# Performance work log

Hardware: AMD Instinct MI355X
Metric: run time of the kernel (lower is better)

Reference implementation:

```python
import jax, jax.numpy as jnp
import numpy as np

B, H, S, D = 4, 8, 2048, 64

def setup_inputs() -> dict:
    key = jax.random.key(0)
    k1, k2 = jax.random.split(key)
    q = jax.random.normal(k1, (B, H, S, D), dtype=jnp.float32)
    kv = jax.random.normal(k2, (B, H, S, D), dtype=jnp.float32)
    mask = jnp.zeros((1, 1, S, S), dtype=jnp.float32)
    return {"q": q, "kv": kv, "mask": mask}

def reference(q, kv, mask):
    # score = q @ kv^T / sqrt(d_k) + mask ; softmax over last dim ; @ kv
    d_k = jnp.asarray(kv.shape[-1], dtype=q.dtype)
    score = jnp.einsum('bhqd,bhkd->bhqk', q, kv) / jnp.sqrt(d_k)
    score = score + mask
    attn = jax.nn.softmax(score, axis=-1)
    out = jnp.einsum('bhqk,bhkd->bhqd', attn, kv)
    return out
```

## Files before the change

### kernel.cpp

```cpp
#include <hip/hip_runtime.h>
#include <hip/hip_bf16.h>
#include <stdint.h>


typedef __bf16 bf16;
typedef __attribute__((ext_vector_type(8))) __bf16 bf16x8;
typedef __attribute__((ext_vector_type(4))) __bf16 bf16x4;
typedef __attribute__((ext_vector_type(4))) float floatx4;
typedef __attribute__((ext_vector_type(16))) float floatx16;
typedef __attribute__((ext_vector_type(4))) int int4v;
typedef __attribute__((ext_vector_type(2))) unsigned int uint2v;

#define SLEN 2048
#define DH   64
#define BR   64
#define BC   64
#define NKT  (SLEN / BC)
#define NEP  (NKT / 2)
#define NQT  (SLEN / BR)
#define BH_N 32
#define LOG2E 1.44269504088896341f

#define CHB_L  1024
#define IMGB_L 8192
#define IMGE_G 4096
#define BUF2   (4 * IMGB_L)

#define AS1 __attribute__((address_space(1)))
#define AS3 __attribute__((address_space(3)))

static __device__ inline void gload_lds16(const void* g, void* l) {
    __builtin_amdgcn_global_load_lds((const AS1 uint32_t*)g, (AS3 uint32_t*)l, 16, 0, 0);
}

static __device__ inline float fexp2(float x) {
    return __builtin_amdgcn_exp2f(x);
}

static_assert(BH_N == NQT, "prep kernel folds bh and qt onto one grid axis");

__global__ __launch_bounds__(256) void kv_prep(
    const float* __restrict__ kv, const float* __restrict__ mask,
    bf16* __restrict__ kvK, bf16* __restrict__ kvT, int* __restrict__ flags)
{
    __shared__ bf16 Tl[64 * 72];
    __shared__ int wany[4];
    const int kt = blockIdx.x, z = blockIdx.y;
    const int t = threadIdx.x;

    float acc = 0.f;
#pragma unroll
    for (int i = 0; i < 4; ++i) {
        int f = i * 256 + t;
        int row = f >> 4, c4 = (f & 15) * 4;
        const float4 v = *(const float4*)(mask + (size_t)(z * BR + row) * SLEN + kt * BC + c4);
        acc = fmaxf(acc, fmaxf(fmaxf(fabsf(v.x), fabsf(v.y)), fmaxf(fabsf(v.z), fabsf(v.w))));
    }
    unsigned long long any = __ballot(acc != 0.f);
    if ((t & 63) == 0) wany[t >> 6] = (any != 0ull) ? 1 : 0;

    const float* src = kv + ((size_t)z * SLEN + kt * BC) * DH;
#pragma unroll
    for (int i = 0; i < 4; ++i) {
        int f = i * 256 + t;
        int key = f >> 4, d4 = (f & 15) * 4;
        float4 v = *(const float4*)(src + (size_t)key * DH + d4);
        bf16x4 b; b[0] = (bf16)v.x; b[1] = (bf16)v.y; b[2] = (bf16)v.z; b[3] = (bf16)v.w;
        *(bf16x4*)&Tl[key * 72 + d4] = b;
    }
    __syncthreads();
    if (t == 0) flags[z * NKT + kt] = wany[0] | wany[1] | wany[2] | wany[3];

    bf16* outK = kvK + ((size_t)z * NKT + kt) * IMGE_G;
#pragma unroll
    for (int i = 0; i < 2; ++i) {
        int G = i * 256 + t;
        int c = G >> 6, L = G & 63, rl = L >> 3, p = L & 7;
        int g = (p - rl - 4 * (c & 1)) & 7, key = 8 * c + rl;
        bf16x8 w = *(const bf16x8*)&Tl[key * 72 + g * 8];
        *(bf16x8*)(outK + (size_t)G * 8) = w;
    }
    bf16* outV = kvT + ((size_t)z * NKT + kt) * IMGE_G;
#pragma unroll
    for (int i = 0; i < 2; ++i) {
        int G = i * 256 + t;
        int c = G >> 6, L = G & 63, dl = L >> 3, p = L & 7;
        int g = (p - dl - 4 * (c & 1)) & 7, d = 8 * c + dl;
        bf16x8 w;
#pragma unroll
        for (int j = 0; j < 8; ++j)
            w[j] = Tl[(8 * g + j) * 72 + d];
        *(bf16x8*)(outV + (size_t)G * 8) = w;
    }
}

__global__ __launch_bounds__(256, 2) void attn_fwd16(
    const float* __restrict__ q, const float* __restrict__ mask,
    const int* __restrict__ flags,
    const bf16* __restrict__ kvK, const bf16* __restrict__ kvT,
    float* __restrict__ out)
{
    __shared__ __align__(16) char smem[2 * BUF2];

    const int bh = blockIdx.x;
    const int qt = blockIdx.y;
    const int q0 = qt * 128;
    const int t = threadIdx.x;
    const int w = t >> 6, lane = t & 63;
    const int r5 = lane & 31, h = lane >> 5;
    const int c3 = r5 >> 3, rl = lane & 7;

    const float qscale = 0.125f * LOG2E;
    bf16x8 qf[4];
    {
        const float* qrow = q + ((size_t)bh * SLEN + q0 + w * 32 + r5) * DH;
#pragma unroll
        for (int s = 0; s < 4; ++s) {
            float4 f0 = *(const float4*)(qrow + 16 * s + 8 * h);
            float4 f1 = *(const float4*)(qrow + 16 * s + 8 * h + 4);
            bf16x8 a;
            a[0] = (bf16)(f0.x * qscale); a[1] = (bf16)(f0.y * qscale);
            a[2] = (bf16)(f0.z * qscale); a[3] = (bf16)(f0.w * qscale);
            a[4] = (bf16)(f1.x * qscale); a[5] = (bf16)(f1.y * qscale);
            a[6] = (bf16)(f1.z * qscale); a[7] = (bf16)(f1.w * qscale);
            qf[s] = a;
        }
    }

    const int fqt = qt * 2 + (w >> 1);
    unsigned fmask;
    {
        int ld = (lane < 32) ? flags[fqt * NKT + lane] : 0;
        fmask = (unsigned)__ballot(ld != 0);
    }

    int addr4[4];
#pragma unroll
    for (int s = 0; s < 4; ++s) {
        int slot = (2 * s + h + rl + 4 * (c3 & 1)) & 7;
        addr4[s] = c3 * 1024 + rl * 128 + slot * 16;
    }

    floatx16 o[2];
#pragma unroll
    for (int dt = 0; dt < 2; ++dt)
#pragma unroll
        for (int i = 0; i < 16; ++i) o[dt][i] = 0.f;
    float l_run = 0.f;

    const bf16* kvKb = kvK + (size_t)bh * NKT * IMGE_G;
    const bf16* kvTb = kvT + (size_t)bh * NKT * IMGE_G;

    auto stage = [&](int t2, char* Bn) {
        const bf16* gK = kvKb + (size_t)t2 * IMGE_G;
        const bf16* gV = kvTb + (size_t)t2 * IMGE_G;
#pragma unroll
        for (int cc = 0; cc < 2; ++cc) {
            const int c = 2 * w + cc;
            gload_lds16(gK + (size_t)c * 512 + lane * 8,          Bn +              c * CHB_L);
            gload_lds16(gV + (size_t)c * 512 + lane * 8,          Bn + IMGB_L +     c * CHB_L);
            gload_lds16(gK + IMGE_G + (size_t)c * 512 + lane * 8, Bn + 2 * IMGB_L + c * CHB_L);
            gload_lds16(gV + IMGE_G + (size_t)c * 512 + lane * 8, Bn + 3 * IMGB_L + c * CHB_L);
        }
    };

    stage(0, smem);

    for (int e = 0; e < NEP; ++e) {
        __syncthreads();

        if (e + 1 < NEP) stage(2 * e + 2, smem + ((e + 1) & 1) * BUF2);

        const char* B = smem + (e & 1) * BUF2;

        floatx16 s[4];
#pragma unroll
        for (int T = 0; T < 4; ++T) {
            const char* Kimg = B + (T >> 1) * (2 * IMGB_L) + (T & 1) * 4096;
            floatx16 acc;
#pragma unroll
            for (int i = 0; i < 16; ++i) acc[i] = 0.f;
#pragma unroll
            for (int ss = 0; ss < 4; ++ss) {
                bf16x8 kf = *(const bf16x8*)(Kimg + addr4[ss]);
                acc = __builtin_amdgcn_mfma_f32_32x32x16_bf16(kf, qf[ss], acc, 0, 0, 0);
            }
            s[T] = acc;
        }

#pragma unroll
        for (int T = 0; T < 4; ++T) {
            if (fmask & (1u << (2 * e + (T >> 1)))) {
                const float* mrow = mask + (size_t)(q0 + w * 32 + r5) * SLEN
                                    + e * 128 + T * 32 + 4 * h;
#pragma unroll
                for (int g4 = 0; g4 < 4; ++g4) {
                    float4 mv = *(const float4*)(mrow + 8 * g4);
                    s[T][4 * g4 + 0] += mv.x * LOG2E;
                    s[T][4 * g4 + 1] += mv.y * LOG2E;
                    s[T][4 * g4 + 2] += mv.z * LOG2E;
                    s[T][4 * g4 + 3] += mv.w * LOG2E;
                }
            }
        }

        float rs = 0.f;
#pragma unroll
        for (int T = 0; T < 4; ++T) {
            float ev[16];
#pragma unroll
            for (int i = 0; i < 16; ++i) ev[i] = fexp2(s[T][i]);
            float r0 = (ev[0] + ev[1]) + (ev[2] + ev[3]);
            float r1 = (ev[4] + ev[5]) + (ev[6] + ev[7]);
            float r2 = (ev[8] + ev[9]) + (ev[10] + ev[11]);
            float r3 = (ev[12] + ev[13]) + (ev[14] + ev[15]);
            rs += (r0 + r1) + (r2 + r3);

            bf16x4 lA = { (bf16)ev[0],  (bf16)ev[1],  (bf16)ev[2],  (bf16)ev[3]  };
            bf16x4 hA = { (bf16)ev[4],  (bf16)ev[5],  (bf16)ev[6],  (bf16)ev[7]  };
            bf16x4 lB = { (bf16)ev[8],  (bf16)ev[9],  (bf16)ev[10], (bf16)ev[11] };
            bf16x4 hB = { (bf16)ev[12], (bf16)ev[13], (bf16)ev[14], (bf16)ev[15] };
            uint2v xA = __builtin_bit_cast(uint2v, lA);
            uint2v yA = __builtin_bit_cast(uint2v, hA);
            uint2v xB = __builtin_bit_cast(uint2v, lB);
            uint2v yB = __builtin_bit_cast(uint2v, hB);
            uint2v sA0 = __builtin_amdgcn_permlane32_swap(xA[0], yA[0], false, false);
            uint2v sA1 = __builtin_amdgcn_permlane32_swap(xA[1], yA[1], false, false);
            uint2v sB0 = __builtin_amdgcn_permlane32_swap(xB[0], yB[0], false, false);
            uint2v sB1 = __builtin_amdgcn_permlane32_swap(xB[1], yB[1], false, false);
            int4v pAi = { (int)sA0[0], (int)sA1[0], (int)sA0[1], (int)sA1[1] };
            int4v pBi = { (int)sB0[0], (int)sB1[0], (int)sB0[1], (int)sB1[1] };
            bf16x8 pfA = __builtin_bit_cast(bf16x8, pAi);
            bf16x8 pfB = __builtin_bit_cast(bf16x8, pBi);

            const char* Vimg = B + IMGB_L + (T >> 1) * (2 * IMGB_L);
            const int uA = 2 * (T & 1), uB = uA + 1;
#pragma unroll
            for (int dt = 0; dt < 2; ++dt) {
                bf16x8 vA = *(const bf16x8*)(Vimg + dt * 4096 + addr4[uA]);
                o[dt] = __builtin_amdgcn_mfma_f32_32x32x16_bf16(vA, pfA, o[dt], 0, 0, 0);
                bf16x8 vB = *(const bf16x8*)(Vimg + dt * 4096 + addr4[uB]);
                o[dt] = __builtin_amdgcn_mfma_f32_32x32x16_bf16(vB, pfB, o[dt], 0, 0, 0);
            }
        }
        l_run += rs;
    }

    float l = l_run + __shfl_xor(l_run, 32);
    const float inv = 1.0f / l;
    float* ob = out + ((size_t)bh * SLEN + q0 + w * 32 + r5) * DH + 4 * h;
#pragma unroll
    for (int dt = 0; dt < 2; ++dt)
#pragma unroll
        for (int k = 0; k < 4; ++k) {
            float4 v;
            v.x = o[dt][4 * k + 0] * inv;
            v.y = o[dt][4 * k + 1] * inv;
            v.z = o[dt][4 * k + 2] * inv;
            v.w = o[dt][4 * k + 3] * inv;
            *(float4*)(ob + dt * 32 + 8 * k) = v;
        }
}

#define LDT 72
__global__ __launch_bounds__(256) void attn_mask_flags(
    const float* __restrict__ mask, int* __restrict__ flags)
{
    const int kt = blockIdx.x, qt = blockIdx.y;
    const int t = threadIdx.x;
    float acc = 0.f;
#pragma unroll
    for (int i = 0; i < 4; ++i) {
        int f = i * 256 + t;
        int row = f >> 4, c4 = (f & 15) * 4;
        const float4 v = *(const float4*)(mask + (size_t)(qt * BR + row) * SLEN + kt * BC + c4);
        acc = fmaxf(acc, fmaxf(fmaxf(fabsf(v.x), fabsf(v.y)), fmaxf(fabsf(v.z), fabsf(v.w))));
    }
    unsigned long long any = __ballot(acc != 0.f);
    __shared__ int wany[4];
    if ((t & 63) == 0) wany[t >> 6] = (any != 0ull) ? 1 : 0;
    __syncthreads();
    if (t == 0) flags[qt * NKT + kt] = wany[0] | wany[1] | wany[2] | wany[3];
}

__global__ __launch_bounds__(256) void attn_fwd(
    const float* __restrict__ q, const float* __restrict__ kv,
    const float* __restrict__ mask, const int* __restrict__ flags,
    float* __restrict__ out)
{
    __shared__ __align__(16) bf16 Kl[BC * LDT];
    __shared__ __align__(16) bf16 Vt[DH * LDT];
    __shared__ __align__(16) bf16 Pl[BR * LDT];

    const int qt = blockIdx.x;
    const int bh = blockIdx.y;
    const int q0 = qt * BR;
    const int t = threadIdx.x;
    const int wave = t >> 6, lane = t & 63;
    const int ln16 = lane & 15, quad = lane >> 4;

    const float qscale = 0.125f * LOG2E;
    bf16x8 aq[2];
    {
        const float* qrow = q + ((size_t)bh * SLEN + q0 + wave * 16 + ln16) * DH;
#pragma unroll
        for (int kc = 0; kc < 2; ++kc) {
            float4 f0 = *(const float4*)(qrow + kc * 32 + quad * 8);
            float4 f1 = *(const float4*)(qrow + kc * 32 + quad * 8 + 4);
            bf16x8 a;
            a[0] = (bf16)(f0.x * qscale); a[1] = (bf16)(f0.y * qscale);
            a[2] = (bf16)(f0.z * qscale); a[3] = (bf16)(f0.w * qscale);
            a[4] = (bf16)(f1.x * qscale); a[5] = (bf16)(f1.y * qscale);
            a[6] = (bf16)(f1.z * qscale); a[7] = (bf16)(f1.w * qscale);
            aq[kc] = a;
        }
    }

    floatx4 o[4];
#pragma unroll
    for (int dt = 0; dt < 4; ++dt) o[dt] = (floatx4){0.f, 0.f, 0.f, 0.f};
    float m_run[4], l_run[4];
#pragma unroll
    for (int r = 0; r < 4; ++r) { m_run[r] = -3.0e38f; l_run[r] = 0.f; }

    const float* kvb = kv + (size_t)bh * SLEN * DH;

    for (int kt = 0; kt < NKT; ++kt) {
        float4 st[4];
        const float* kvt = kvb + (size_t)kt * BC * DH;
#pragma unroll
        for (int i = 0; i < 4; ++i) {
            int f = i * 256 + t;
            st[i] = *(const float4*)(kvt + (size_t)f * 4);
        }
        __syncthreads();
#pragma unroll
        for (int i = 0; i < 4; ++i) {
            int f = i * 256 + t;
            int key = f >> 4, d4 = (f & 15) * 4;
            bf16 b0 = (bf16)st[i].x, b1 = (bf16)st[i].y, b2 = (bf16)st[i].z, b3 = (bf16)st[i].w;
            *(bf16x4*)&Kl[key * LDT + d4] = (bf16x4){b0, b1, b2, b3};
            Vt[(d4 + 0) * LDT + key] = b0;
            Vt[(d4 + 1) * LDT + key] = b1;
            Vt[(d4 + 2) * LDT + key] = b2;
            Vt[(d4 + 3) * LDT + key] = b3;
        }
        __syncthreads();

        floatx4 s[4];
#pragma unroll
        for (int nt = 0; nt < 4; ++nt) {
            s[nt] = (floatx4){0.f, 0.f, 0.f, 0.f};
#pragma unroll
            for (int kc = 0; kc < 2; ++kc) {
                bf16x8 bk = *(const bf16x8*)&Kl[(ln16 + 16 * nt) * LDT + kc * 32 + quad * 8];
                s[nt] = __builtin_amdgcn_mfma_f32_16x16x32_bf16(aq[kc], bk, s[nt], 0, 0, 0);
            }
        }

        if (!flags || flags[qt * NKT + kt]) {
            const float* mrow = mask + (size_t)(q0 + quad * 4) * SLEN + kt * BC + ln16;
#pragma unroll
            for (int r = 0; r < 4; ++r)
#pragma unroll
                for (int nt = 0; nt < 4; ++nt)
                    s[nt][r] += mrow[(size_t)r * SLEN + nt * 16] * LOG2E;
        }

#pragma unroll
        for (int r = 0; r < 4; ++r) {
            float mx = fmaxf(fmaxf(s[0][r], s[1][r]), fmaxf(s[2][r], s[3][r]));
            mx = fmaxf(mx, __shfl_xor(mx, 1));
            mx = fmaxf(mx, __shfl_xor(mx, 2));
            mx = fmaxf(mx, __shfl_xor(mx, 4));
            mx = fmaxf(mx, __shfl_xor(mx, 8));
            float mnew = fmaxf(m_run[r], mx);
            float alpha = exp2f(m_run[r] - mnew);
            m_run[r] = mnew;
            float rs = 0.f;
#pragma unroll
            for (int nt = 0; nt < 4; ++nt) {
                float p = exp2f(s[nt][r] - mnew);
                s[nt][r] = p;
                rs += p;
            }
            rs += __shfl_xor(rs, 1);
            rs += __shfl_xor(rs, 2);
            rs += __shfl_xor(rs, 4);
            rs += __shfl_xor(rs, 8);
            l_run[r] = l_run[r] * alpha + rs;
#pragma unroll
            for (int dt = 0; dt < 4; ++dt) o[dt][r] *= alpha;
        }

#pragma unroll
        for (int nt = 0; nt < 4; ++nt)
#pragma unroll
            for (int r = 0; r < 4; ++r)
                Pl[(wave * 16 + quad * 4 + r) * LDT + ln16 + 16 * nt] = (bf16)s[nt][r];

#pragma unroll
        for (int kc2 = 0; kc2 < 2; ++kc2) {
            bf16x8 pfr = *(const bf16x8*)&Pl[(wave * 16 + ln16) * LDT + kc2 * 32 + quad * 8];
#pragma unroll
            for (int dt = 0; dt < 4; ++dt) {
                bf16x8 vfr = *(const bf16x8*)&Vt[(ln16 + 16 * dt) * LDT + kc2 * 32 + quad * 8];
                o[dt] = __builtin_amdgcn_mfma_f32_16x16x32_bf16(pfr, vfr, o[dt], 0, 0, 0);
            }
        }
    }

#pragma unroll
    for (int r = 0; r < 4; ++r) {
        float inv = 1.0f / l_run[r];
        int qrow = q0 + wave * 16 + quad * 4 + r;
        float* orow = out + ((size_t)bh * SLEN + qrow) * DH;
#pragma unroll
        for (int dt = 0; dt < 4; ++dt)
            orow[ln16 + 16 * dt] = o[dt][r] * inv;
    }
}

extern "C" void kernel_launch(void* const* d_in, const int* in_sizes, int n_in,
                              void* d_out, int out_size, void* d_ws, size_t ws_size,
                              hipStream_t stream)
{
    const float* q    = (const float*)d_in[0];
    const float* kv   = (const float*)d_in[1];
    const float* mask = (const float*)d_in[2];
    float* out = (float*)d_out;

    const size_t kvKoff = 4096;
    const size_t kvToff = kvKoff + (size_t)BH_N * NKT * IMGE_G * 2;
    const size_t need   = kvToff + (size_t)BH_N * NKT * IMGE_G * 2;

    if (ws_size >= need) {
        int*  flags = (int*)d_ws;
        bf16* kvK   = (bf16*)((char*)d_ws + kvKoff);
        bf16* kvT   = (bf16*)((char*)d_ws + kvToff);
        kv_prep<<<dim3(NKT, BH_N), 256, 0, stream>>>(kv, mask, kvK, kvT, flags);
        attn_fwd16<<<dim3(BH_N, SLEN / 128), 256, 0, stream>>>(q, mask, flags, kvK, kvT, out);
    } else {
        int* flags = nullptr;
        if (ws_size >= (size_t)NQT * NKT * sizeof(int)) {
            flags = (int*)d_ws;
            attn_mask_flags<<<dim3(NKT, NQT), 256, 0, stream>>>(mask, flags);
        }
        attn_fwd<<<dim3(NQT, BH_N), 256, 0, stream>>>(q, kv, mask, flags, out);
    }
}
```

Baseline: 133.1 us.

## Split key tiles across warp pairs, each warp covering 64 query rows, reduce via LDS

Each warp now handles 64 query rows (two 32-row groups) but only one of the two 64-key tiles per stage, instead of 32 query rows over both key tiles. Every K and V fragment read from LDS now feeds two MFMAs, halving LDS read traffic per MFMA. The partial outputs and row sums of the two key-half warps are combined through shared memory at the end. The cost is more accumulator registers (four output tiles plus doubled scores) under the 2-blocks-per-SM launch bound, and an extra LDS reduction with barriers.

```diff
diff --git a/kernel.cpp b/kernel.cpp
--- a/kernel.cpp
+++ b/kernel.cpp
@@ -94,7 +94,7 @@
     }
 }
 
-__global__ __launch_bounds__(256, 2) void attn_fwd16(
+__global__ __launch_bounds__(256, 2) void attn_fwd17(
     const float* __restrict__ q, const float* __restrict__ mask,
     const int* __restrict__ flags,
     const bf16* __restrict__ kvK, const bf16* __restrict__ kvT,
@@ -107,13 +107,15 @@
     const int q0 = qt * 128;
     const int t = threadIdx.x;
     const int w = t >> 6, lane = t & 63;
+    const int kh = w & 1, qh = w >> 1;
     const int r5 = lane & 31, h = lane >> 5;
     const int c3 = r5 >> 3, rl = lane & 7;
 
     const float qscale = 0.125f * LOG2E;
-    bf16x8 qf[4];
-    {
-        const float* qrow = q + ((size_t)bh * SLEN + q0 + w * 32 + r5) * DH;
+    bf16x8 qf[2][4];
+#pragma unroll
+    for (int g = 0; g < 2; ++g) {
+        const float* qrow = q + ((size_t)bh * SLEN + q0 + qh * 64 + g * 32 + r5) * DH;
 #pragma unroll
         for (int s = 0; s < 4; ++s) {
             float4 f0 = *(const float4*)(qrow + 16 * s + 8 * h);
@@ -123,11 +125,11 @@
             a[2] = (bf16)(f0.z * qscale); a[3] = (bf16)(f0.w * qscale);
             a[4] = (bf16)(f1.x * qscale); a[5] = (bf16)(f1.y * qscale);
             a[6] = (bf16)(f1.z * qscale); a[7] = (bf16)(f1.w * qscale);
-            qf[s] = a;
-        }
-    }
-
-    const int fqt = qt * 2 + (w >> 1);
+            qf[g][s] = a;
+        }
+    }
+
+    const int fqt = qt * 2 + qh;
     unsigned fmask;
     {
         int ld = (lane < 32) ? flags[fqt * NKT + lane] : 0;
@@ -141,12 +143,14 @@
         addr4[s] = c3 * 1024 + rl * 128 + slot * 16;
     }
 
-    floatx16 o[2];
-#pragma unroll
-    for (int dt = 0; dt < 2; ++dt)
-#pragma unroll
-        for (int i = 0; i < 16; ++i) o[dt][i] = 0.f;
-    float l_run = 0.f;
+    floatx16 o[2][2];
+#pragma unroll
+    for (int g = 0; g < 2; ++g)
+#pragma unroll
+        for (int dt = 0; dt < 2; ++dt)
+#pragma unroll
+            for (int i = 0; i < 16; ++i) o[g][dt][i] = 0.f;
+    float l_run[2] = {0.f, 0.f};
 
     const bf16* kvKb = kvK + (size_t)bh * NKT * IMGE_G;
     const bf16* kvTb = kvT + (size_t)bh * NKT * IMGE_G;
@@ -171,95 +175,142 @@
 
         if (e + 1 < NEP) stage(2 * e + 2, smem + ((e + 1) & 1) * BUF2);
 
-        const char* B = smem + (e & 1) * BUF2;
-
-        floatx16 s[4];
-#pragma unroll
-        for (int T = 0; T < 4; ++T) {
-            const char* Kimg = B + (T >> 1) * (2 * IMGB_L) + (T & 1) * 4096;
-            floatx16 acc;
-#pragma unroll
-            for (int i = 0; i < 16; ++i) acc[i] = 0.f;
+        const char* B    = smem + (e & 1) * BUF2;
+        const char* Kimg = B + kh * (2 * IMGB_L);
+        const char* Vimg = B + IMGB_L + kh * (2 * IMGB_L);
+        const int   ktile = 2 * e + kh;
+        const bool  domask = (fmask >> ktile) & 1u;
+
+#pragma unroll
+        for (int T = 0; T < 2; ++T) {
+            floatx16 s0, s1;
+#pragma unroll
+            for (int i = 0; i < 16; ++i) { s0[i] = 0.f; s1[i] = 0.f; }
 #pragma unroll
             for (int ss = 0; ss < 4; ++ss) {
-                bf16x8 kf = *(const bf16x8*)(Kimg + addr4[ss]);
-                acc = __builtin_amdgcn_mfma_f32_32x32x16_bf16(kf, qf[ss], acc, 0, 0, 0);
-            }
-            s[T] = acc;
-        }
-
-#pragma unroll
-        for (int T = 0; T < 4; ++T) {
-            if (fmask & (1u << (2 * e + (T >> 1)))) {
-                const float* mrow = mask + (size_t)(q0 + w * 32 + r5) * SLEN
-                                    + e * 128 + T * 32 + 4 * h;
+                bf16x8 kf = *(const bf16x8*)(Kimg + T * 4096 + addr4[ss]);
+                s0 = __builtin_amdgcn_mfma_f32_32x32x16_bf16(kf, qf[0][ss], s0, 0, 0, 0);
+                s1 = __builtin_amdgcn_mfma_f32_32x32x16_bf16(kf, qf[1][ss], s1, 0, 0, 0);
+            }
+
+            if (domask) {
+                const float* m0 = mask + (size_t)(q0 + qh * 64 + r5) * SLEN
+                                  + ktile * 64 + T * 32 + 4 * h;
+                const float* m1 = m0 + (size_t)32 * SLEN;
 #pragma unroll
                 for (int g4 = 0; g4 < 4; ++g4) {
-                    float4 mv = *(const float4*)(mrow + 8 * g4);
-                    s[T][4 * g4 + 0] += mv.x * LOG2E;
-                    s[T][4 * g4 + 1] += mv.y * LOG2E;
-                    s[T][4 * g4 + 2] += mv.z * LOG2E;
-                    s[T][4 * g4 + 3] += mv.w * LOG2E;
+                    float4 a = *(const float4*)(m0 + 8 * g4);
+                    float4 b = *(const float4*)(m1 + 8 * g4);
+                    s0[4 * g4 + 0] += a.x * LOG2E; s0[4 * g4 + 1] += a.y * LOG2E;
+                    s0[4 * g4 + 2] += a.z * LOG2E; s0[4 * g4 + 3] += a.w * LOG2E;
+                    s1[4 * g4 + 0] += b.x * LOG2E; s1[4 * g4 + 1] += b.y * LOG2E;
+                    s1[4 * g4 + 2] += b.z * LOG2E; s1[4 * g4 + 3] += b.w * LOG2E;
                 }
             }
-        }
-
-        float rs = 0.f;
-#pragma unroll
-        for (int T = 0; T < 4; ++T) {
-            float ev[16];
-#pragma unroll
-            for (int i = 0; i < 16; ++i) ev[i] = fexp2(s[T][i]);
-            float r0 = (ev[0] + ev[1]) + (ev[2] + ev[3]);
-            float r1 = (ev[4] + ev[5]) + (ev[6] + ev[7]);
-            float r2 = (ev[8] + ev[9]) + (ev[10] + ev[11]);
-            float r3 = (ev[12] + ev[13]) + (ev[14] + ev[15]);
-            rs += (r0 + r1) + (r2 + r3);
-
-            bf16x4 lA = { (bf16)ev[0],  (bf16)ev[1],  (bf16)ev[2],  (bf16)ev[3]  };
-            bf16x4 hA = { (bf16)ev[4],  (bf16)ev[5],  (bf16)ev[6],  (bf16)ev[7]  };
-            bf16x4 lB = { (bf16)ev[8],  (bf16)ev[9],  (bf16)ev[10], (bf16)ev[11] };
-            bf16x4 hB = { (bf16)ev[12], (bf16)ev[13], (bf16)ev[14], (bf16)ev[15] };
-            uint2v xA = __builtin_bit_cast(uint2v, lA);
-            uint2v yA = __builtin_bit_cast(uint2v, hA);
-            uint2v xB = __builtin_bit_cast(uint2v, lB);
-            uint2v yB = __builtin_bit_cast(uint2v, hB);
-            uint2v sA0 = __builtin_amdgcn_permlane32_swap(xA[0], yA[0], false, false);
-            uint2v sA1 = __builtin_amdgcn_permlane32_swap(xA[1], yA[1], false, false);
-            uint2v sB0 = __builtin_amdgcn_permlane32_swap(xB[0], yB[0], false, false);
-            uint2v sB1 = __builtin_amdgcn_permlane32_swap(xB[1], yB[1], false, false);
-            int4v pAi = { (int)sA0[0], (int)sA1[0], (int)sA0[1], (int)sA1[1] };
-            int4v pBi = { (int)sB0[0], (int)sB1[0], (int)sB0[1], (int)sB1[1] };
-            bf16x8 pfA = __builtin_bit_cast(bf16x8, pAi);
-            bf16x8 pfB = __builtin_bit_cast(bf16x8, pBi);
-
-            const char* Vimg = B + IMGB_L + (T >> 1) * (2 * IMGB_L);
-            const int uA = 2 * (T & 1), uB = uA + 1;
+
+            float ev0[16], ev1[16];
+#pragma unroll
+            for (int i = 0; i < 16; ++i) { ev0[i] = fexp2(s0[i]); ev1[i] = fexp2(s1[i]); }
+            l_run[0] += ((ev0[0] + ev0[1]) + (ev0[2] + ev0[3]))
+                      + ((ev0[4] + ev0[5]) + (ev0[6] + ev0[7]))
+                      + ((ev0[8] + ev0[9]) + (ev0[10] + ev0[11]))
+                      + ((ev0[12] + ev0[13]) + (ev0[14] + ev0[15]));
+            l_run[1] += ((ev1[0] + ev1[1]) + (ev1[2] + ev1[3]))
+                      + ((ev1[4] + ev1[5]) + (ev1[6] + ev1[7]))
+                      + ((ev1[8] + ev1[9]) + (ev1[10] + ev1[11]))
+                      + ((ev1[12] + ev1[13]) + (ev1[14] + ev1[15]));
+
+            bf16x8 pf0A, pf0B, pf1A, pf1B;
+            {
+                bf16x4 lA = { (bf16)ev0[0],  (bf16)ev0[1],  (bf16)ev0[2],  (bf16)ev0[3]  };
+                bf16x4 hA = { (bf16)ev0[4],  (bf16)ev0[5],  (bf16)ev0[6],  (bf16)ev0[7]  };
+                bf16x4 lB = { (bf16)ev0[8],  (bf16)ev0[9],  (bf16)ev0[10], (bf16)ev0[11] };
+                bf16x4 hB = { (bf16)ev0[12], (bf16)ev0[13], (bf16)ev0[14], (bf16)ev0[15] };
+                uint2v xA = __builtin_bit_cast(uint2v, lA);
+                uint2v yA = __builtin_bit_cast(uint2v, hA);
+                uint2v xB = __builtin_bit_cast(uint2v, lB);
+                uint2v yB = __builtin_bit_cast(uint2v, hB);
+                uint2v sA0 = __builtin_amdgcn_permlane32_swap(xA[0], yA[0], false, false);
+                uint2v sA1 = __builtin_amdgcn_permlane32_swap(xA[1], yA[1], false, false);
+                uint2v sB0 = __builtin_amdgcn_permlane32_swap(xB[0], yB[0], false, false);
+                uint2v sB1 = __builtin_amdgcn_permlane32_swap(xB[1], yB[1], false, false);
+                int4v pAi = { (int)sA0[0], (int)sA1[0], (int)sA0[1], (int)sA1[1] };
+                int4v pBi = { (int)sB0[0], (int)sB1[0], (int)sB0[1], (int)sB1[1] };
+                pf0A = __builtin_bit_cast(bf16x8, pAi);
+                pf0B = __builtin_bit_cast(bf16x8, pBi);
+            }
+            {
+                bf16x4 lA = { (bf16)ev1[0],  (bf16)ev1[1],  (bf16)ev1[2],  (bf16)ev1[3]  };
+                bf16x4 hA = { (bf16)ev1[4],  (bf16)ev1[5],  (bf16)ev1[6],  (bf16)ev1[7]  };
+                bf16x4 lB = { (bf16)ev1[8],  (bf16)ev1[9],  (bf16)ev1[10], (bf16)ev1[11] };
+                bf16x4 hB = { (bf16)ev1[12], (bf16)ev1[13], (bf16)ev1[14], (bf16)ev1[15] };
+                uint2v xA = __builtin_bit_cast(uint2v, lA);
+                uint2v yA = __builtin_bit_cast(uint2v, hA);
+                uint2v xB = __builtin_bit_cast(uint2v, lB);
+                uint2v yB = __builtin_bit_cast(uint2v, hB);
+                uint2v sA0 = __builtin_amdgcn_permlane32_swap(xA[0], yA[0], false, false);
+                uint2v sA1 = __builtin_amdgcn_permlane32_swap(xA[1], yA[1], false, false);
+                uint2v sB0 = __builtin_amdgcn_permlane32_swap(xB[0], yB[0], false, false);
+                uint2v sB1 = __builtin_amdgcn_permlane32_swap(xB[1], yB[1], false, false);
+                int4v pAi = { (int)sA0[0], (int)sA1[0], (int)sA0[1], (int)sA1[1] };
+                int4v pBi = { (int)sB0[0], (int)sB1[0], (int)sB0[1], (int)sB1[1] };
+                pf1A = __builtin_bit_cast(bf16x8, pAi);
+                pf1B = __builtin_bit_cast(bf16x8, pBi);
+            }
+
+            const int uA = 2 * T, uB = 2 * T + 1;
 #pragma unroll
             for (int dt = 0; dt < 2; ++dt) {
                 bf16x8 vA = *(const bf16x8*)(Vimg + dt * 4096 + addr4[uA]);
-                o[dt] = __builtin_amdgcn_mfma_f32_32x32x16_bf16(vA, pfA, o[dt], 0, 0, 0);
                 bf16x8 vB = *(const bf16x8*)(Vimg + dt * 4096 + addr4[uB]);
-                o[dt] = __builtin_amdgcn_mfma_f32_32x32x16_bf16(vB, pfB, o[dt], 0, 0, 0);
-            }
-        }
-        l_run += rs;
-    }
-
-    float l = l_run + __shfl_xor(l_run, 32);
-    const float inv = 1.0f / l;
-    float* ob = out + ((size_t)bh * SLEN + q0 + w * 32 + r5) * DH + 4 * h;
-#pragma unroll
-    for (int dt = 0; dt < 2; ++dt)
-#pragma unroll
-        for (int k = 0; k < 4; ++k) {
-            float4 v;
-            v.x = o[dt][4 * k + 0] * inv;
-            v.y = o[dt][4 * k + 1] * inv;
-            v.z = o[dt][4 * k + 2] * inv;
-            v.w = o[dt][4 * k + 3] * inv;
-            *(float4*)(ob + dt * 32 + 8 * k) = v;
-        }
+                o[0][dt] = __builtin_amdgcn_mfma_f32_32x32x16_bf16(vA, pf0A, o[0][dt], 0, 0, 0);
+                o[0][dt] = __builtin_amdgcn_mfma_f32_32x32x16_bf16(vB, pf0B, o[0][dt], 0, 0, 0);
+                o[1][dt] = __builtin_amdgcn_mfma_f32_32x32x16_bf16(vA, pf1A, o[1][dt], 0, 0, 0);
+                o[1][dt] = __builtin_amdgcn_mfma_f32_32x32x16_bf16(vB, pf1B, o[1][dt], 0, 0, 0);
+            }
+        }
+    }
+
+    __syncthreads();
+    float* Obuf = (float*)smem;
+    float* Lbuf = (float*)(smem + 32768);
+    if (kh == 1) {
+#pragma unroll
+        for (int g = 0; g < 2; ++g) {
+#pragma unroll
+            for (int dt = 0; dt < 2; ++dt)
+#pragma unroll
+                for (int k = 0; k < 4; ++k) {
+                    float4 v;
+                    v.x = o[g][dt][4 * k + 0]; v.y = o[g][dt][4 * k + 1];
+                    v.z = o[g][dt][4 * k + 2]; v.w = o[g][dt][4 * k + 3];
+                    *(float4*)(Obuf + ((size_t)(((qh * 2 + g) * 2 + dt) * 4 + k) * 64 + lane) * 4) = v;
+                }
+            Lbuf[(qh * 2 + g) * 64 + lane] = l_run[g];
+        }
+    }
+    __syncthreads();
+    if (kh == 0) {
+#pragma unroll
+        for (int g = 0; g < 2; ++g) {
+            float lsum = l_run[g] + Lbuf[(qh * 2 + g) * 64 + lane];
+            float l = lsum + __shfl_xor(lsum, 32);
+            float inv = 1.f / l;
+            float* ob = out + ((size_t)bh * SLEN + q0 + qh * 64 + g * 32 + r5) * DH + 4 * h;
+#pragma unroll
+            for (int dt = 0; dt < 2; ++dt)
+#pragma unroll
+                for (int k = 0; k < 4; ++k) {
+                    float4 p = *(const float4*)(Obuf + ((size_t)(((qh * 2 + g) * 2 + dt) * 4 + k) * 64 + lane) * 4);
+                    float4 v;
+                    v.x = (o[g][dt][4 * k + 0] + p.x) * inv;
+                    v.y = (o[g][dt][4 * k + 1] + p.y) * inv;
+                    v.z = (o[g][dt][4 * k + 2] + p.z) * inv;
+                    v.w = (o[g][dt][4 * k + 3] + p.w) * inv;
+                    *(float4*)(ob + dt * 32 + 8 * k) = v;
+                }
+        }
+    }
 }
 
 #define LDT 72
@@ -439,7 +490,7 @@
         bf16* kvK   = (bf16*)((char*)d_ws + kvKoff);
         bf16* kvT   = (bf16*)((char*)d_ws + kvToff);
         kv_prep<<<dim3(NKT, BH_N), 256, 0, stream>>>(kv, mask, kvK, kvT, flags);
-        attn_fwd16<<<dim3(BH_N, SLEN / 128), 256, 0, stream>>>(q, mask, flags, kvK, kvT, out);
+        attn_fwd17<<<dim3(BH_N, SLEN / 128), 256, 0, stream>>>(q, mask, flags, kvK, kvT, out);
     } else {
         int* flags = nullptr;
         if (ws_size >= (size_t)NQT * NKT * sizeof(int)) {
```

Measured after the change: 133.7 us. Within noise of the previous version (+0.5%).

## Split KV range across two wave groups, load fragments directly from global

Applied to the files above, without the earlier changes.

The attention kernel now uses 512 threads, with two groups of four waves each covering half of the key tiles for the same query rows. It drops the LDS double-buffered staging and instead reads K/V fragments straight from global memory, using a new prep layout that matches the MFMA operand order. Partial outputs and row sums are combined through shared memory at the end. The aim is more waves in flight to hide latency and no LDS staging or barriers per tile, at the cost of uncoalesced-by-LDS global reads relying on cache and an extra reduction step.

```diff
diff --git a/kernel.cpp b/kernel.cpp
--- a/kernel.cpp
+++ b/kernel.cpp
@@ -16,22 +16,14 @@
 #define BR   64
 #define BC   64
 #define NKT  (SLEN / BC)
-#define NEP  (NKT / 2)
 #define NQT  (SLEN / BR)
 #define BH_N 32
 #define LOG2E 1.44269504088896341f
 
-#define CHB_L  1024
-#define IMGB_L 8192
 #define IMGE_G 4096
-#define BUF2   (4 * IMGB_L)
 
 #define AS1 __attribute__((address_space(1)))
 #define AS3 __attribute__((address_space(3)))
-
-static __device__ inline void gload_lds16(const void* g, void* l) {
-    __builtin_amdgcn_global_load_lds((const AS1 uint32_t*)g, (AS3 uint32_t*)l, 16, 0, 0);
-}
 
 static __device__ inline float fexp2(float x) {
     return __builtin_amdgcn_exp2f(x);
@@ -75,45 +67,46 @@
 #pragma unroll
     for (int i = 0; i < 2; ++i) {
         int G = i * 256 + t;
-        int c = G >> 6, L = G & 63, rl = L >> 3, p = L & 7;
-        int g = (p - rl - 4 * (c & 1)) & 7, key = 8 * c + rl;
-        bf16x8 w = *(const bf16x8*)&Tl[key * 72 + g * 8];
+        int u = G >> 8, ss = (G >> 6) & 3, ln = G & 63;
+        int key = u * 32 + (ln & 31), d0 = 16 * ss + 8 * (ln >> 5);
+        bf16x8 w = *(const bf16x8*)&Tl[key * 72 + d0];
         *(bf16x8*)(outK + (size_t)G * 8) = w;
     }
     bf16* outV = kvT + ((size_t)z * NKT + kt) * IMGE_G;
 #pragma unroll
     for (int i = 0; i < 2; ++i) {
         int G = i * 256 + t;
-        int c = G >> 6, L = G & 63, dl = L >> 3, p = L & 7;
-        int g = (p - dl - 4 * (c & 1)) & 7, d = 8 * c + dl;
+        int dt = G >> 8, u = (G >> 7) & 1, ff = (G >> 6) & 1, ln = G & 63;
+        int d = dt * 32 + (ln & 31), kb = u * 32 + 16 * ff + 8 * (ln >> 5);
         bf16x8 w;
 #pragma unroll
         for (int j = 0; j < 8; ++j)
-            w[j] = Tl[(8 * g + j) * 72 + d];
+            w[j] = Tl[(kb + j) * 72 + d];
         *(bf16x8*)(outV + (size_t)G * 8) = w;
     }
 }
 
-__global__ __launch_bounds__(256, 2) void attn_fwd16(
+__global__ __launch_bounds__(512, 2) void attn_fwd19(
     const float* __restrict__ q, const float* __restrict__ mask,
     const int* __restrict__ flags,
     const bf16* __restrict__ kvK, const bf16* __restrict__ kvT,
     float* __restrict__ out)
 {
-    __shared__ __align__(16) char smem[2 * BUF2];
+    __shared__ __align__(16) float Obuf[4 * 2 * 4 * 64 * 4];
+    __shared__ float Lbuf[4 * 64];
 
     const int bh = blockIdx.x;
     const int qt = blockIdx.y;
     const int q0 = qt * 128;
     const int t = threadIdx.x;
     const int w = t >> 6, lane = t & 63;
+    const int qg = w & 3, kh = w >> 2;
     const int r5 = lane & 31, h = lane >> 5;
-    const int c3 = r5 >> 3, rl = lane & 7;
 
     const float qscale = 0.125f * LOG2E;
     bf16x8 qf[4];
     {
-        const float* qrow = q + ((size_t)bh * SLEN + q0 + w * 32 + r5) * DH;
+        const float* qrow = q + ((size_t)bh * SLEN + q0 + qg * 32 + r5) * DH;
 #pragma unroll
         for (int s = 0; s < 4; ++s) {
             float4 f0 = *(const float4*)(qrow + 16 * s + 8 * h);
@@ -127,20 +120,13 @@
         }
     }
 
-    const int fqt = qt * 2 + (w >> 1);
+    const int fqt = qt * 2 + (qg >> 1);
     unsigned fmask;
     {
         int ld = (lane < 32) ? flags[fqt * NKT + lane] : 0;
         fmask = (unsigned)__ballot(ld != 0);
     }
 
-    int addr4[4];
-#pragma unroll
-    for (int s = 0; s < 4; ++s) {
-        int slot = (2 * s + h + rl + 4 * (c3 & 1)) & 7;
-        addr4[s] = c3 * 1024 + rl * 128 + slot * 16;
-    }
-
     floatx16 o[2];
 #pragma unroll
     for (int dt = 0; dt < 2; ++dt)
@@ -148,78 +134,62 @@
         for (int i = 0; i < 16; ++i) o[dt][i] = 0.f;
     float l_run = 0.f;
 
-    const bf16* kvKb = kvK + (size_t)bh * NKT * IMGE_G;
-    const bf16* kvTb = kvT + (size_t)bh * NKT * IMGE_G;
-
-    auto stage = [&](int t2, char* Bn) {
-        const bf16* gK = kvKb + (size_t)t2 * IMGE_G;
-        const bf16* gV = kvTb + (size_t)t2 * IMGE_G;
-#pragma unroll
-        for (int cc = 0; cc < 2; ++cc) {
-            const int c = 2 * w + cc;
-            gload_lds16(gK + (size_t)c * 512 + lane * 8,          Bn +              c * CHB_L);
-            gload_lds16(gV + (size_t)c * 512 + lane * 8,          Bn + IMGB_L +     c * CHB_L);
-            gload_lds16(gK + IMGE_G + (size_t)c * 512 + lane * 8, Bn + 2 * IMGB_L + c * CHB_L);
-            gload_lds16(gV + IMGE_G + (size_t)c * 512 + lane * 8, Bn + 3 * IMGB_L + c * CHB_L);
-        }
-    };
-
-    stage(0, smem);
-
-    for (int e = 0; e < NEP; ++e) {
-        __syncthreads();
-
-        if (e + 1 < NEP) stage(2 * e + 2, smem + ((e + 1) & 1) * BUF2);
-
-        const char* B = smem + (e & 1) * BUF2;
-
-        floatx16 s[4];
-#pragma unroll
-        for (int T = 0; T < 4; ++T) {
-            const char* Kimg = B + (T >> 1) * (2 * IMGB_L) + (T & 1) * 4096;
-            floatx16 acc;
-#pragma unroll
-            for (int i = 0; i < 16; ++i) acc[i] = 0.f;
-#pragma unroll
-            for (int ss = 0; ss < 4; ++ss) {
-                bf16x8 kf = *(const bf16x8*)(Kimg + addr4[ss]);
-                acc = __builtin_amdgcn_mfma_f32_32x32x16_bf16(kf, qf[ss], acc, 0, 0, 0);
-            }
-            s[T] = acc;
-        }
-
-#pragma unroll
-        for (int T = 0; T < 4; ++T) {
-            if (fmask & (1u << (2 * e + (T >> 1)))) {
-                const float* mrow = mask + (size_t)(q0 + w * 32 + r5) * SLEN
-                                    + e * 128 + T * 32 + 4 * h;
+    const char* Kb = (const char*)(kvK + (size_t)bh * NKT * IMGE_G) + lane * 16;
+    const char* Vb = (const char*)(kvT + (size_t)bh * NKT * IMGE_G) + lane * 16;
+
+    for (int e = 0; e < 16; ++e) {
+        const int kt = kh * 16 + e;
+        const char* Kt = Kb + (size_t)kt * 8192;
+        const char* Vt = Vb + (size_t)kt * 8192;
+        const bool dm = (fmask >> kt) & 1u;
+
+#pragma unroll
+        for (int u = 0; u < 2; ++u) {
+            floatx16 s;
+#pragma unroll
+            for (int i = 0; i < 16; ++i) s[i] = 0.f;
+            {
+                const char* Ku = Kt + u * 4096;
+                bf16x8 kf0 = *(const bf16x8*)(Ku);
+                bf16x8 kf1 = *(const bf16x8*)(Ku + 1024);
+                bf16x8 kf2 = *(const bf16x8*)(Ku + 2048);
+                bf16x8 kf3 = *(const bf16x8*)(Ku + 3072);
+                s = __builtin_amdgcn_mfma_f32_32x32x16_bf16(kf0, qf[0], s, 0, 0, 0);
+                s = __builtin_amdgcn_mfma_f32_32x32x16_bf16(kf1, qf[1], s, 0, 0, 0);
+                s = __builtin_amdgcn_mfma_f32_32x32x16_bf16(kf2, qf[2], s, 0, 0, 0);
+                s = __builtin_amdgcn_mfma_f32_32x32x16_bf16(kf3, qf[3], s, 0, 0, 0);
+            }
+
+            if (dm) {
+                const float* mrow = mask + (size_t)(q0 + qg * 32 + r5) * SLEN
+                                    + kt * 64 + u * 32 + 4 * h;
 #pragma unroll
                 for (int g4 = 0; g4 < 4; ++g4) {
                     float4 mv = *(const float4*)(mrow + 8 * g4);
-                    s[T][4 * g4 + 0] += mv.x * LOG2E;
-                    s[T][4 * g4 + 1] += mv.y * LOG2E;
-                    s[T][4 * g4 + 2] += mv.z * LOG2E;
-                    s[T][4 * g4 + 3] += mv.w * LOG2E;
+                    s[4 * g4 + 0] += mv.x * LOG2E;
+                    s[4 * g4 + 1] += mv.y * LOG2E;
+                    s[4 * g4 + 2] += mv.z * LOG2E;
+                    s[4 * g4 + 3] += mv.w * LOG2E;
                 }
             }
-        }
-
-        float rs = 0.f;
-#pragma unroll
-        for (int T = 0; T < 4; ++T) {
-            float ev[16];
-#pragma unroll
-            for (int i = 0; i < 16; ++i) ev[i] = fexp2(s[T][i]);
-            float r0 = (ev[0] + ev[1]) + (ev[2] + ev[3]);
-            float r1 = (ev[4] + ev[5]) + (ev[6] + ev[7]);
-            float r2 = (ev[8] + ev[9]) + (ev[10] + ev[11]);
-            float r3 = (ev[12] + ev[13]) + (ev[14] + ev[15]);
-            rs += (r0 + r1) + (r2 + r3);
-
-            bf16x4 lA = { (bf16)ev[0],  (bf16)ev[1],  (bf16)ev[2],  (bf16)ev[3]  };
-            bf16x4 hA = { (bf16)ev[4],  (bf16)ev[5],  (bf16)ev[6],  (bf16)ev[7]  };
-            bf16x4 lB = { (bf16)ev[8],  (bf16)ev[9],  (bf16)ev[10], (bf16)ev[11] };
-            bf16x4 hB = { (bf16)ev[12], (bf16)ev[13], (bf16)ev[14], (bf16)ev[15] };
+
+            const char* Vu = Vt + u * 2048;
+            bf16x8 v00 = *(const bf16x8*)(Vu);
+            bf16x8 v01 = *(const bf16x8*)(Vu + 1024);
+            bf16x8 v10 = *(const bf16x8*)(Vu + 4096);
+            bf16x8 v11 = *(const bf16x8*)(Vu + 4096 + 1024);
+
+#pragma unroll
+            for (int i = 0; i < 16; ++i) s[i] = fexp2(s[i]);
+            l_run += ((s[0] + s[1]) + (s[2] + s[3]))
+                   + ((s[4] + s[5]) + (s[6] + s[7]))
+                   + ((s[8] + s[9]) + (s[10] + s[11]))
+                   + ((s[12] + s[13]) + (s[14] + s[15]));
+
+            bf16x4 lA = { (bf16)s[0],  (bf16)s[1],  (bf16)s[2],  (bf16)s[3]  };
+            bf16x4 hA = { (bf16)s[4],  (bf16)s[5],  (bf16)s[6],  (bf16)s[7]  };
+            bf16x4 lB = { (bf16)s[8],  (bf16)s[9],  (bf16)s[10], (bf16)s[11] };
+            bf16x4 hB = { (bf16)s[12], (bf16)s[13], (bf16)s[14], (bf16)s[15] };
             uint2v xA = __builtin_bit_cast(uint2v, lA);
             uint2v yA = __builtin_bit_cast(uint2v, hA);
             uint2v xB = __builtin_bit_cast(uint2v, lB);
@@ -233,33 +203,45 @@
             bf16x8 pfA = __builtin_bit_cast(bf16x8, pAi);
             bf16x8 pfB = __builtin_bit_cast(bf16x8, pBi);
 
-            const char* Vimg = B + IMGB_L + (T >> 1) * (2 * IMGB_L);
-            const int uA = 2 * (T & 1), uB = uA + 1;
-#pragma unroll
-            for (int dt = 0; dt < 2; ++dt) {
-                bf16x8 vA = *(const bf16x8*)(Vimg + dt * 4096 + addr4[uA]);
-                o[dt] = __builtin_amdgcn_mfma_f32_32x32x16_bf16(vA, pfA, o[dt], 0, 0, 0);
-                bf16x8 vB = *(const bf16x8*)(Vimg + dt * 4096 + addr4[uB]);
-                o[dt] = __builtin_amdgcn_mfma_f32_32x32x16_bf16(vB, pfB, o[dt], 0, 0, 0);
-            }
-        }
-        l_run += rs;
-    }
-
-    float l = l_run + __shfl_xor(l_run, 32);
-    const float inv = 1.0f / l;
-    float* ob = out + ((size_t)bh * SLEN + q0 + w * 32 + r5) * DH + 4 * h;
-#pragma unroll
-    for (int dt = 0; dt < 2; ++dt)
-#pragma unroll
-        for (int k = 0; k < 4; ++k) {
-            float4 v;
-            v.x = o[dt][4 * k + 0] * inv;
-            v.y = o[dt][4 * k + 1] * inv;
-            v.z = o[dt][4 * k + 2] * inv;
-            v.w = o[dt][4 * k + 3] * inv;
-            *(float4*)(ob + dt * 32 + 8 * k) = v;
-        }
+            o[0] = __builtin_amdgcn_mfma_f32_32x32x16_bf16(v00, pfA, o[0], 0, 0, 0);
+            o[0] = __builtin_amdgcn_mfma_f32_32x32x16_bf16(v01, pfB, o[0], 0, 0, 0);
+            o[1] = __builtin_amdgcn_mfma_f32_32x32x16_bf16(v10, pfA, o[1], 0, 0, 0);
+            o[1] = __builtin_amdgcn_mfma_f32_32x32x16_bf16(v11, pfB, o[1], 0, 0, 0);
+        }
+    }
+
+    __syncthreads();
+    if (kh == 1) {
+#pragma unroll
+        for (int dt = 0; dt < 2; ++dt)
+#pragma unroll
+            for (int k = 0; k < 4; ++k) {
+                float4 v;
+                v.x = o[dt][4 * k + 0]; v.y = o[dt][4 * k + 1];
+                v.z = o[dt][4 * k + 2]; v.w = o[dt][4 * k + 3];
+                *(float4*)(Obuf + ((size_t)((qg * 2 + dt) * 4 + k) * 64 + lane) * 4) = v;
+            }
+        Lbuf[qg * 64 + lane] = l_run;
+    }
+    __syncthreads();
+    if (kh == 0) {
+        float lsum = l_run + Lbuf[qg * 64 + lane];
+        float l = lsum + __shfl_xor(lsum, 32);
+        float inv = 1.f / l;
+        float* ob = out + ((size_t)bh * SLEN + q0 + qg * 32 + r5) * DH + 4 * h;
+#pragma unroll
+        for (int dt = 0; dt < 2; ++dt)
+#pragma unroll
+            for (int k = 0; k < 4; ++k) {
+                float4 p = *(const float4*)(Obuf + ((size_t)((qg * 2 + dt) * 4 + k) * 64 + lane) * 4);
+                float4 v;
+                v.x = (o[dt][4 * k + 0] + p.x) * inv;
+                v.y = (o[dt][4 * k + 1] + p.y) * inv;
+                v.z = (o[dt][4 * k + 2] + p.z) * inv;
+                v.w = (o[dt][4 * k + 3] + p.w) * inv;
+                *(float4*)(ob + dt * 32 + 8 * k) = v;
+            }
+    }
 }
 
 #define LDT 72
@@ -439,7 +421,7 @@
         bf16* kvK   = (bf16*)((char*)d_ws + kvKoff);
         bf16* kvT   = (bf16*)((char*)d_ws + kvToff);
         kv_prep<<<dim3(NKT, BH_N), 256, 0, stream>>>(kv, mask, kvK, kvT, flags);
-        attn_fwd16<<<dim3(BH_N, SLEN / 128), 256, 0, stream>>>(q, mask, flags, kvK, kvT, out);
+        attn_fwd19<<<dim3(BH_N, SLEN / 128), 512, 0, stream>>>(q, mask, flags, kvK, kvT, out);
     } else {
         int* flags = nullptr;
         if (ws_size >= (size_t)NQT * NKT * sizeof(int)) {
```

After: 136.4 us. +2.5%, slower.
